# Performance work log

Measured on AMD Instinct MI355X. Metric: run time of the kernel, lower is better.

Reference implementation:

```python
import jax, jax.numpy as jnp
import numpy as np

N_NODES = 4096
HIDDEN = 64
N_REL = 8
N_LAYERS = 2


def setup_inputs() -> dict:
    key = jax.random.key(0)
    k0, k1, k2, k3, k4 = jax.random.split(key, 5)
    node_embed = jax.random.normal(k0, (N_NODES + 1, HIDDEN), dtype=jnp.float32)
    w_self = jax.random.normal(k1, (N_LAYERS, HIDDEN, HIDDEN), dtype=jnp.float32) * 0.02
    w_rel = jax.random.normal(k2, (N_LAYERS, N_REL, HIDDEN, HIDDEN), dtype=jnp.float32) * 0.02
    # dense per-relation adjacency buffer [R, N, N]
    rel_adj = jax.random.uniform(k3, (N_REL, N_NODES, N_NODES), dtype=jnp.float32)
    keyword_ids = jax.random.randint(k4, (64, 32), 0, N_NODES + 1)  # pad id == N_NODES
    return {"node_embed": node_embed, "w_self": w_self, "w_rel": w_rel,
            "rel_adj": rel_adj, "keyword_ids": keyword_ids}


def reference(node_embed, w_self, w_rel, rel_adj, keyword_ids):
    num_nodes = rel_adj.shape[1]
    h = node_embed[:num_nodes]  # [N, D]
    for l in range(w_self.shape[0]):
        out = h @ w_self[l]                                   # self loop [N, D]
        msg = jnp.einsum('rnm,md->rnd', rel_adj, h)           # per-relation aggregation
        out = out + jnp.einsum('rnd,rde->ne', msg, w_rel[l])  # per-relation projection, summed over r
        h = jax.nn.relu(out)
    pad = jnp.zeros((1, h.shape[1]), dtype=h.dtype)
    full_plus_pad = jnp.concatenate([h, pad], axis=0)  # [N+1, D]
    return full_plus_pad[keyword_ids]                  # [B, K, D]
```

## Files before the change

kernel.cpp:

```cpp
#include <hip/hip_runtime.h>

#define N_NODES 4096
#define HID 64
#define NREL 8

typedef float f32x4 __attribute__((ext_vector_type(4)));
typedef short s16x8 __attribute__((ext_vector_type(8)));

__device__ __forceinline__ short f2bf(float f) {
    union { float f; unsigned u; } v; v.f = f;
    unsigned r = v.u + 0x7fffu + ((v.u >> 16) & 1u);
    return (short)(r >> 16);
}

__global__ __launch_bounds__(256) void proj_kernel(
    const float* __restrict__ h, const float* __restrict__ w_self_l,
    const float* __restrict__ w_rel_l, float* __restrict__ S,
    unsigned short* __restrict__ BT)
{
    __shared__ float hs[64][65];
    __shared__ float wt[64][64];
    const int tid = threadIdx.x;
    const int mb = blockIdx.x;
    const int p = blockIdx.y;
    const float* w = (p < 8) ? (w_rel_l + p * 64 * 64) : w_self_l;

    #pragma unroll
    for (int i = 0; i < 4; ++i) {
        int idx4 = tid + 256 * i;
        int row = idx4 >> 4, c = idx4 & 15;
        float4 v = *((const float4*)(h + (size_t)(mb * 64 + row) * HID) + c);
        hs[row][c * 4 + 0] = v.x; hs[row][c * 4 + 1] = v.y;
        hs[row][c * 4 + 2] = v.z; hs[row][c * 4 + 3] = v.w;
    }
    #pragma unroll
    for (int i = 0; i < 4; ++i) {
        int idx4 = tid + 256 * i;
        ((float4*)wt)[idx4] = ((const float4*)w)[idx4];
    }
    __syncthreads();

    const int m = tid & 63;
    const int eb = (tid >> 6) * 16;
    float acc[16];
    #pragma unroll
    for (int j = 0; j < 16; ++j) acc[j] = 0.f;

    #pragma unroll 4
    for (int d = 0; d < 64; ++d) {
        float hv = hs[m][d];
        const float4* wr = (const float4*)&wt[d][eb];
        float4 w0 = wr[0], w1 = wr[1], w2 = wr[2], w3 = wr[3];
        acc[0]  += hv * w0.x; acc[1]  += hv * w0.y; acc[2]  += hv * w0.z; acc[3]  += hv * w0.w;
        acc[4]  += hv * w1.x; acc[5]  += hv * w1.y; acc[6]  += hv * w1.z; acc[7]  += hv * w1.w;
        acc[8]  += hv * w2.x; acc[9]  += hv * w2.y; acc[10] += hv * w2.z; acc[11] += hv * w2.w;
        acc[12] += hv * w3.x; acc[13] += hv * w3.y; acc[14] += hv * w3.z; acc[15] += hv * w3.w;
    }

    if (p < 8) {
        #pragma unroll
        for (int j = 0; j < 16; ++j)
            BT[(size_t)(p * 64 + eb + j) * N_NODES + mb * 64 + m] = (unsigned short)f2bf(acc[j]);
    } else {
        #pragma unroll
        for (int j = 0; j < 16; ++j)
            S[(size_t)(mb * 64 + m) * HID + eb + j] = acc[j];
    }
}

__global__ __launch_bounds__(256) void gemm_kernel(
    const float* __restrict__ A, const unsigned short* __restrict__ BT,
    float* __restrict__ msgacc)
{
    __shared__ float At[64][68];
    __shared__ unsigned short Bt[64][72];

    const int tid = threadIdx.x;
    const int gid = blockIdx.x;
    const int r = gid & 7;
    const int rb = gid >> 3;
    const float* Ar = A + ((size_t)r * N_NODES + (size_t)rb * 64) * N_NODES;
    const unsigned short* BTr = BT + (size_t)r * 64 * N_NODES;

    const int wave = tid >> 6, lane = tid & 63;
    const int quad = lane >> 4, l16 = lane & 15;

    f32x4 acc[4];
    #pragma unroll
    for (int nb = 0; nb < 4; ++nb) acc[nb] = (f32x4){0.f, 0.f, 0.f, 0.f};

    for (int kb = 0; kb < 64; ++kb) {
        #pragma unroll
        for (int i = 0; i < 4; ++i) {
            int idx4 = tid + 256 * i;
            int row = idx4 >> 4, c = idx4 & 15;
            float4 v = *((const float4*)(Ar + (size_t)row * N_NODES + kb * 64) + c);
            *(float4*)&At[row][c * 4] = v;
        }
        #pragma unroll
        for (int i = 0; i < 2; ++i) {
            int idx4 = tid + 256 * i;
            int row = idx4 >> 3, c = idx4 & 7;
            float4 v = *((const float4*)(BTr + (size_t)row * N_NODES + kb * 64) + c);
            *(float4*)&Bt[row][c * 8] = v;
        }
        __syncthreads();

        const int arow = wave * 16 + l16;
        #pragma unroll
        for (int kk = 0; kk < 64; kk += 32) {
            const float* ap = &At[arow][kk + quad * 8];
            float4 a0 = *(const float4*)ap;
            float4 a1 = *(const float4*)(ap + 4);
            s16x8 af;
            af[0] = f2bf(a0.x); af[1] = f2bf(a0.y); af[2] = f2bf(a0.z); af[3] = f2bf(a0.w);
            af[4] = f2bf(a1.x); af[5] = f2bf(a1.y); af[6] = f2bf(a1.z); af[7] = f2bf(a1.w);
            #pragma unroll
            for (int nb = 0; nb < 4; ++nb) {
                s16x8 bfr = *(const s16x8*)&Bt[nb * 16 + l16][kk + quad * 8];
                acc[nb] = __builtin_amdgcn_mfma_f32_16x16x32_bf16(af, bfr, acc[nb], 0, 0, 0);
            }
        }
        __syncthreads();
    }

    #pragma unroll
    for (int nb = 0; nb < 4; ++nb) {
        #pragma unroll
        for (int i = 0; i < 4; ++i) {
            int row = rb * 64 + wave * 16 + quad * 4 + i;
            int col = nb * 16 + l16;
            atomicAdd(&msgacc[(size_t)row * HID + col], acc[nb][i]);
        }
    }
}

__global__ __launch_bounds__(256) void relu_kernel(
    const float* __restrict__ S, const float* __restrict__ msg, float* __restrict__ hout)
{
    int i = blockIdx.x * 256 + threadIdx.x;
    hout[i] = fmaxf(S[i] + msg[i], 0.f);
}

__global__ __launch_bounds__(256) void gather_kernel(
    const float* __restrict__ h2, const int* __restrict__ kw, float* __restrict__ out)
{
    int e = blockIdx.x * 256 + threadIdx.x;
    int ki = e >> 6, d = e & 63;
    int id = kw[ki];
    out[e] = ((unsigned)id < (unsigned)N_NODES) ? h2[(size_t)id * HID + d] : 0.f;
}

extern "C" void kernel_launch(void* const* d_in, const int* in_sizes, int n_in,
                              void* d_out, int out_size, void* d_ws, size_t ws_size,
                              hipStream_t stream) {
    const float* node_embed = (const float*)d_in[0];
    const float* w_self     = (const float*)d_in[1];
    const float* w_rel      = (const float*)d_in[2];
    const float* rel_adj    = (const float*)d_in[3];
    const int*   kw         = (const int*)d_in[4];
    float* out = (float*)d_out;

    float* msgacc = (float*)d_ws;
    float* S      = msgacc + N_NODES * HID;
    float* h1     = S + N_NODES * HID;
    float* h2     = h1 + N_NODES * HID;
    unsigned short* BT = (unsigned short*)(h2 + N_NODES * HID);

    const float* hin = node_embed;
    float* houts[2] = {h1, h2};
    for (int l = 0; l < 2; ++l) {
        hipMemsetAsync(msgacc, 0, (size_t)N_NODES * HID * sizeof(float), stream);
        proj_kernel<<<dim3(64, 9), 256, 0, stream>>>(
            hin, w_self + (size_t)l * 64 * 64, w_rel + (size_t)l * 8 * 64 * 64, S, BT);
        gemm_kernel<<<512, 256, 0, stream>>>(rel_adj, BT, msgacc);
        relu_kernel<<<1024, 256, 0, stream>>>(S, msgacc, houts[l]);
        hin = houts[l];
    }
    gather_kernel<<<512, 256, 0, stream>>>(h2, kw, out);
}
```

Measured before the change: 1.012 ms.

## Stream adjacency directly to MFMA registers, split K, replace atomics with partial buffers

The GEMM kernel now drops its LDS staging and syncthreads. Each lane loads its A fragment straight from global memory with nontemporal loads and reads B fragments directly from the bf16 projected buffer. The K dimension is split in two, doubling the grid to 1024 blocks. Each (relation, k-split) pair writes its partial result to its own buffer instead of doing atomicAdds, which also removes the memset. The relu kernel then sums 16 partials with float4 loads. The aim is better occupancy and bandwidth on the 512MB adjacency stream. The cost is uncoalesced per-lane strided global loads, with no data reuse through LDS, plus extra partial-buffer traffic.

```diff
diff --git a/kernel.cpp b/kernel.cpp
--- a/kernel.cpp
+++ b/kernel.cpp
@@ -2,7 +2,7 @@
 
 #define N_NODES 4096
 #define HID 64
-#define NREL 8
+#define NH (N_NODES * HID)
 
 typedef float f32x4 __attribute__((ext_vector_type(4)));
 typedef short s16x8 __attribute__((ext_vector_type(8)));
@@ -16,7 +16,7 @@
 __global__ __launch_bounds__(256) void proj_kernel(
     const float* __restrict__ h, const float* __restrict__ w_self_l,
     const float* __restrict__ w_rel_l, float* __restrict__ S,
-    unsigned short* __restrict__ BT)
+    short* __restrict__ BT)
 {
     __shared__ float hs[64][65];
     __shared__ float wt[64][64];
@@ -60,7 +60,7 @@
     if (p < 8) {
         #pragma unroll
         for (int j = 0; j < 16; ++j)
-            BT[(size_t)(p * 64 + eb + j) * N_NODES + mb * 64 + m] = (unsigned short)f2bf(acc[j]);
+            BT[(size_t)(p * 64 + eb + j) * N_NODES + mb * 64 + m] = f2bf(acc[j]);
     } else {
         #pragma unroll
         for (int j = 0; j < 16; ++j)
@@ -69,68 +69,46 @@
 }
 
 __global__ __launch_bounds__(256) void gemm_kernel(
-    const float* __restrict__ A, const unsigned short* __restrict__ BT,
-    float* __restrict__ msgacc)
+    const float* __restrict__ A, const short* __restrict__ BT,
+    float* __restrict__ msg)
 {
-    __shared__ float At[64][68];
-    __shared__ unsigned short Bt[64][72];
-
     const int tid = threadIdx.x;
     const int gid = blockIdx.x;
-    const int r = gid & 7;
-    const int rb = gid >> 3;
-    const float* Ar = A + ((size_t)r * N_NODES + (size_t)rb * 64) * N_NODES;
-    const unsigned short* BTr = BT + (size_t)r * 64 * N_NODES;
-
+    const int r  = gid & 7;
+    const int rb = (gid >> 3) & 63;
+    const int ks = gid >> 9;
     const int wave = tid >> 6, lane = tid & 63;
     const int quad = lane >> 4, l16 = lane & 15;
+
+    const int row = rb * 64 + wave * 16 + l16;
+    const float* arow = A + ((size_t)r * N_NODES + row) * N_NODES + ks * 2048 + quad * 8;
+    const short* bbase = BT + ((size_t)r * 64 + l16) * N_NODES + ks * 2048 + quad * 8;
 
     f32x4 acc[4];
     #pragma unroll
     for (int nb = 0; nb < 4; ++nb) acc[nb] = (f32x4){0.f, 0.f, 0.f, 0.f};
 
-    for (int kb = 0; kb < 64; ++kb) {
+    #pragma unroll 2
+    for (int k = 0; k < 2048; k += 32) {
+        f32x4 a0 = __builtin_nontemporal_load((const f32x4*)(arow + k));
+        f32x4 a1 = __builtin_nontemporal_load((const f32x4*)(arow + k + 4));
+        s16x8 af;
+        af[0] = f2bf(a0[0]); af[1] = f2bf(a0[1]); af[2] = f2bf(a0[2]); af[3] = f2bf(a0[3]);
+        af[4] = f2bf(a1[0]); af[5] = f2bf(a1[1]); af[6] = f2bf(a1[2]); af[7] = f2bf(a1[3]);
         #pragma unroll
-        for (int i = 0; i < 4; ++i) {
-            int idx4 = tid + 256 * i;
-            int row = idx4 >> 4, c = idx4 & 15;
-            float4 v = *((const float4*)(Ar + (size_t)row * N_NODES + kb * 64) + c);
-            *(float4*)&At[row][c * 4] = v;
+        for (int nb = 0; nb < 4; ++nb) {
+            s16x8 bfr = *(const s16x8*)(bbase + (size_t)nb * 16 * N_NODES + k);
+            acc[nb] = __builtin_amdgcn_mfma_f32_16x16x32_bf16(af, bfr, acc[nb], 0, 0, 0);
         }
-        #pragma unroll
-        for (int i = 0; i < 2; ++i) {
-            int idx4 = tid + 256 * i;
-            int row = idx4 >> 3, c = idx4 & 7;
-            float4 v = *((const float4*)(BTr + (size_t)row * N_NODES + kb * 64) + c);
-            *(float4*)&Bt[row][c * 8] = v;
-        }
-        __syncthreads();
-
-        const int arow = wave * 16 + l16;
-        #pragma unroll
-        for (int kk = 0; kk < 64; kk += 32) {
-            const float* ap = &At[arow][kk + quad * 8];
-            float4 a0 = *(const float4*)ap;
-            float4 a1 = *(const float4*)(ap + 4);
-            s16x8 af;
-            af[0] = f2bf(a0.x); af[1] = f2bf(a0.y); af[2] = f2bf(a0.z); af[3] = f2bf(a0.w);
-            af[4] = f2bf(a1.x); af[5] = f2bf(a1.y); af[6] = f2bf(a1.z); af[7] = f2bf(a1.w);
-            #pragma unroll
-            for (int nb = 0; nb < 4; ++nb) {
-                s16x8 bfr = *(const s16x8*)&Bt[nb * 16 + l16][kk + quad * 8];
-                acc[nb] = __builtin_amdgcn_mfma_f32_16x16x32_bf16(af, bfr, acc[nb], 0, 0, 0);
-            }
-        }
-        __syncthreads();
     }
 
+    float* mo = msg + ((size_t)(r * 2 + ks)) * NH;
     #pragma unroll
     for (int nb = 0; nb < 4; ++nb) {
         #pragma unroll
         for (int i = 0; i < 4; ++i) {
-            int row = rb * 64 + wave * 16 + quad * 4 + i;
-            int col = nb * 16 + l16;
-            atomicAdd(&msgacc[(size_t)row * HID + col], acc[nb][i]);
+            int orow = rb * 64 + wave * 16 + quad * 4 + i;
+            mo[(size_t)orow * HID + nb * 16 + l16] = acc[nb][i];
         }
     }
 }
@@ -139,7 +117,16 @@
     const float* __restrict__ S, const float* __restrict__ msg, float* __restrict__ hout)
 {
     int i = blockIdx.x * 256 + threadIdx.x;
-    hout[i] = fmaxf(S[i] + msg[i], 0.f);
+    float4 s = ((const float4*)S)[i];
+    #pragma unroll
+    for (int p = 0; p < 16; ++p) {
+        float4 m = ((const float4*)(msg + (size_t)p * NH))[i];
+        s.x += m.x; s.y += m.y; s.z += m.z; s.w += m.w;
+    }
+    float4 o;
+    o.x = fmaxf(s.x, 0.f); o.y = fmaxf(s.y, 0.f);
+    o.z = fmaxf(s.z, 0.f); o.w = fmaxf(s.w, 0.f);
+    ((float4*)hout)[i] = o;
 }
 
 __global__ __launch_bounds__(256) void gather_kernel(
@@ -161,20 +148,19 @@
     const int*   kw         = (const int*)d_in[4];
     float* out = (float*)d_out;
 
-    float* msgacc = (float*)d_ws;
-    float* S      = msgacc + N_NODES * HID;
-    float* h1     = S + N_NODES * HID;
-    float* h2     = h1 + N_NODES * HID;
-    unsigned short* BT = (unsigned short*)(h2 + N_NODES * HID);
+    float* msg = (float*)d_ws;
+    float* S   = msg + 16 * NH;
+    float* h1  = S + NH;
+    float* h2  = h1 + NH;
+    short* BT  = (short*)(h2 + NH);
 
     const float* hin = node_embed;
     float* houts[2] = {h1, h2};
     for (int l = 0; l < 2; ++l) {
-        hipMemsetAsync(msgacc, 0, (size_t)N_NODES * HID * sizeof(float), stream);
         proj_kernel<<<dim3(64, 9), 256, 0, stream>>>(
             hin, w_self + (size_t)l * 64 * 64, w_rel + (size_t)l * 8 * 64 * 64, S, BT);
-        gemm_kernel<<<512, 256, 0, stream>>>(rel_adj, BT, msgacc);
-        relu_kernel<<<1024, 256, 0, stream>>>(S, msgacc, houts[l]);
+        gemm_kernel<<<1024, 256, 0, stream>>>(rel_adj, BT, msg);
+        relu_kernel<<<256, 256, 0, stream>>>(S, msg, houts[l]);
         hin = houts[l];
     }
     gather_kernel<<<512, 256, 0, stream>>>(h2, kw, out);
```

Result: faster. 975.3 us (-3.7%).
